# Kernel optimization log

Measured on AMD Instinct MI355X. Metric: run time of the kernel, lower is better.

## Reference

```python
import jax, jax.numpy as jnp
import numpy as np

N, D, OUT, E, K = 65536, 256, 256, 8, 2  # tokens, input_dim, output_dim, num_experts, top-k


def setup_inputs() -> dict:
    key = jax.random.key(0)
    k1, k2, k3, k4 = jax.random.split(key, 4)
    x = jax.random.normal(k1, (N, D), dtype=jnp.float32)
    # xavier_normal-like init for the gate
    w_gate = jax.random.normal(k2, (D, E), dtype=jnp.float32) * np.float32(np.sqrt(2.0 / (D + E)))
    # PWLayer params stacked over experts: bias init zeros, weight std 0.02
    expert_bias = jax.random.normal(k3, (E, D), dtype=jnp.float32) * 0.01
    expert_weight = jax.random.normal(k4, (E, OUT, D), dtype=jnp.float32) * 0.02
    return {"x": x, "w_gate": w_gate, "expert_bias": expert_bias, "expert_weight": expert_weight}


def reference(x, w_gate, expert_bias, expert_weight):
    # --- noisy_top_k_gating (eval mode: clean logits only) ---
    logits = x @ w_gate                                   # [N, E]
    top_v, top_i = jax.lax.top_k(logits, K)               # [N, K]
    sparse_logits = jnp.full_like(logits, -jnp.inf)
    rows = jnp.arange(logits.shape[0])[:, None]           # [N, 1]
    sparse_logits = sparse_logits.at[rows, top_i].set(top_v)
    gates = jax.nn.softmax(sparse_logits, axis=-1)        # [N, E], zeros off the top-k
    # --- dense all-expert PWLayer pass: (x - bias_e) @ W_e^T ---
    centered = x[:, None, :] - expert_bias[None, :, :]    # [N, E, D]
    expert_stack = jnp.einsum('ned,eod->neo', centered, expert_weight)  # [N, E, OUT]
    # --- gated combine ---
    return jnp.einsum('ne,neo->no', gates, expert_stack)  # [N, OUT]
```

## Files before the change

### kernel.cpp

```cpp
#include <hip/hip_runtime.h>
#include <hip/hip_bf16.h>
#include <math.h>

#define N_TOK 65536
#define DIM   256
#define NEXP  8

using frag_ab = __attribute__((ext_vector_type(8))) short;
using frag_cd = __attribute__((ext_vector_type(4))) float;

__device__ __forceinline__ unsigned short f2bf(float f) {
  unsigned u = __float_as_uint(f);
  u += 0x7FFFu + ((u >> 16) & 1u);
  return (unsigned short)(u >> 16);
}

__device__ __forceinline__ void gl2lds16(const unsigned short* g, unsigned short* l) {
  __builtin_amdgcn_global_load_lds(
      (const __attribute__((address_space(1))) void*)g,
      (__attribute__((address_space(3))) void*)l, 16, 0, 0);
}


__global__ __launch_bounds__(256) void k_prep(
    const float* __restrict__ w,
    const float* __restrict__ bias,
    unsigned short* __restrict__ Wb,
    float* __restrict__ c,
    int* __restrict__ meta) {
  int tid = threadIdx.x;
  int wid = (blockIdx.x * 256 + tid) >> 6;
  int lane = tid & 63;
  int e = wid >> 8, o = wid & 255;
  const float* wr = w + (size_t)(e * 256 + o) * DIM + lane * 4;
  float4 wv = *(const float4*)wr;
  const float* br = bias + e * DIM + lane * 4;
  float4 bv = *(const float4*)br;
  float s = wv.x * bv.x + wv.y * bv.y + wv.z * bv.z + wv.w * bv.w;
  #pragma unroll
  for (int m = 1; m < 64; m <<= 1) s += __shfl_xor(s, m, 64);
  if (lane == 0) c[e * 256 + o] = s;
  ushort4 h; h.x = f2bf(wv.x); h.y = f2bf(wv.y); h.z = f2bf(wv.z); h.w = f2bf(wv.w);
  *(ushort4*)(Wb + (size_t)e * 65536 + (size_t)(lane >> 1) * 2048 + o * 8 + (lane & 1) * 4) = h;
  if (blockIdx.x == 0 && tid < 192) meta[tid] = 0;
}

__global__ __launch_bounds__(256) void k_gating(
    const float* __restrict__ x,
    const float* __restrict__ wg,
    unsigned short* __restrict__ xb,
    int* __restrict__ routeE,
    float* __restrict__ routeG,
    int* __restrict__ meta) {
  __shared__ double swg[DIM * NEXP];
  __shared__ float  chunk[64 * 35];
  __shared__ int    hcnt[64];
  int tid = threadIdx.x;
  int tok0 = blockIdx.x * 64;
  int tk = tid >> 2, sub = tid & 3;

  for (int i = tid; i < DIM * NEXP; i += 256) swg[i] = (double)wg[i];
  if (tid < 64) hcnt[tid] = 0;

  double p[NEXP];
  #pragma unroll
  for (int e = 0; e < NEXP; e++) p[e] = 0.0;

  int f0 = tid, f1 = 256 + tid;
  int r0 = f0 >> 3, c40 = (f0 & 7) * 4;
  int r1 = f1 >> 3, c41 = (f1 & 7) * 4;
  const float* xs0 = x + (size_t)(tok0 + r0) * DIM + c40;
  const float* xs1 = x + (size_t)(tok0 + r1) * DIM + c41;
  unsigned short* xd0 = xb + (size_t)(tok0 + r0) * DIM + c40;
  unsigned short* xd1 = xb + (size_t)(tok0 + r1) * DIM + c41;

  float4 v0 = *(const float4*)(xs0);
  float4 v1 = *(const float4*)(xs1);

  for (int dc = 0; dc < 8; dc++) {
    __syncthreads();
    {
      ushort4 h0; h0.x = f2bf(v0.x); h0.y = f2bf(v0.y); h0.z = f2bf(v0.z); h0.w = f2bf(v0.w);
      ushort4 h1; h1.x = f2bf(v1.x); h1.y = f2bf(v1.y); h1.z = f2bf(v1.z); h1.w = f2bf(v1.w);
      *(ushort4*)(xd0 + dc * 32) = h0;
      *(ushort4*)(xd1 + dc * 32) = h1;
      float* d0 = &chunk[r0 * 35 + c40];
      d0[0] = v0.x; d0[1] = v0.y; d0[2] = v0.z; d0[3] = v0.w;
      float* d1 = &chunk[r1 * 35 + c41];
      d1[0] = v1.x; d1[1] = v1.y; d1[2] = v1.z; d1[3] = v1.w;
    }
    float4 n0 = make_float4(0.f, 0.f, 0.f, 0.f);
    float4 n1 = make_float4(0.f, 0.f, 0.f, 0.f);
    if (dc < 7) {
      n0 = *(const float4*)(xs0 + (dc + 1) * 32);
      n1 = *(const float4*)(xs1 + (dc + 1) * 32);
    }
    __syncthreads();
    #pragma unroll
    for (int c8 = 0; c8 < 8; c8++) {
      int cc = c8 * 4 + sub;
      double xv = (double)chunk[tk * 35 + cc];
      const double* wrow = &swg[(dc * 32 + cc) * NEXP];
      #pragma unroll
      for (int e = 0; e < NEXP; e++) p[e] += xv * wrow[e];
    }
    v0 = n0; v1 = n1;
  }

  #pragma unroll
  for (int e = 0; e < NEXP; e++) {
    p[e] += __shfl_xor(p[e], 1, 64);
    p[e] += __shfl_xor(p[e], 2, 64);
  }

  if (sub == 0) {
    int i1 = 0; double v1d = p[0];
    #pragma unroll
    for (int e = 1; e < NEXP; e++) { if (p[e] > v1d) { v1d = p[e]; i1 = e; } }
    int i2 = -1; double v2d = -1e300;
    #pragma unroll
    for (int e = 0; e < NEXP; e++) { if (e != i1 && p[e] > v2d) { v2d = p[e]; i2 = e; } }
    double t = exp(v2d - v1d);
    float g1 = (float)(1.0 / (1.0 + t));
    float g2 = 1.0f - g1;

    int n = tok0 + tk;
    routeE[n] = i1 | (i2 << 8);
    *(float2*)(routeG + 2 * (size_t)n) = make_float2(g1, g2);
    int a = i1 < i2 ? i1 : i2, b = i1 < i2 ? i2 : i1;
    atomicAdd(&hcnt[a * 8 + b], 1);
  }
  __syncthreads();
  if (tid < 64) atomicAdd(&meta[tid], hcnt[tid]);
}

__global__ void k_scan(int* __restrict__ meta) {
  if (threadIdx.x == 0) {
    int run = 0;
    for (int p = 0; p < 64; p++) {
      meta[64 + p] = run; meta[128 + p] = run;
      run += ((meta[p] + 63) >> 6) << 6;
    }
  }
}

__global__ __launch_bounds__(1024) void k_scatter(
    const int* __restrict__ routeE, const float* __restrict__ routeG,
    int* __restrict__ meta,
    int* __restrict__ srcTok, float* __restrict__ srcGA, float* __restrict__ srcGB) {
  __shared__ int cnt[64], bse[64];
  int tid = threadIdx.x;
  if (tid < 64) cnt[tid] = 0;
  __syncthreads();
  int n = blockIdx.x * 1024 + tid;
  int ep = routeE[n];
  int e1 = ep & 255, e2 = ep >> 8;
  float2 g = *(const float2*)(routeG + 2 * (size_t)n);
  int a = e1 < e2 ? e1 : e2, b = e1 < e2 ? e2 : e1;
  float ga = e1 < e2 ? g.x : g.y;
  float gb = e1 < e2 ? g.y : g.x;
  int pid = a * 8 + b;
  int r = atomicAdd(&cnt[pid], 1);
  __syncthreads();
  if (tid < 64) bse[tid] = atomicAdd(&meta[128 + tid], cnt[tid]);
  __syncthreads();
  int p = bse[pid] + r;
  srcTok[p] = n; srcGA[p] = ga; srcGB[p] = gb;
}

__global__ __launch_bounds__(512, 4) void k_gemm_pair(
    const unsigned short* __restrict__ xb,
    const unsigned short* __restrict__ Wb,
    const int* __restrict__ meta,
    const int* __restrict__ srcTok,
    const float* __restrict__ srcGA, const float* __restrict__ srcGB,
    const float* __restrict__ c,
    float* __restrict__ out) {
  __shared__ unsigned short sA[4][64 * 64];
  __shared__ int   sTok[64];
  __shared__ float sGAs[64], sGBs[64];
  __shared__ float sCorA[256], sCorB[256];
  int tid = threadIdx.x;

  int rem = blockIdx.x, pid = 0, ne = 0;
  for (pid = 0; pid < 64; pid++) {
    ne = meta[pid];
    int tiles = (ne + 63) >> 6;
    if (rem < tiles) break;
    rem -= tiles;
  }
  if (pid == 64) return;
  int ea = pid >> 3, eb = pid & 7;
  int mt = rem;
  int slot0 = meta[64 + pid] + mt * 64;

  if (tid < 64) {
    int idx = mt * 64 + tid;
    bool v = idx < ne;
    sTok[tid]  = v ? srcTok[slot0 + tid] : 0;
    sGAs[tid]  = v ? srcGA[slot0 + tid] : 0.f;
    sGBs[tid]  = v ? srcGB[slot0 + tid] : 1.f;
  } else if (tid >= 128 && tid < 192) {
    ((float4*)sCorA)[tid - 128] = ((const float4*)(c + ea * 256))[tid - 128];
  } else if (tid >= 192 && tid < 256) {
    ((float4*)sCorB)[tid - 192] = ((const float4*)(c + eb * 256))[tid - 192];
  }
  __syncthreads();

  int w = tid >> 6, lane = tid & 63;
  int lrow = lane >> 3, lchk = lane & 7;

  {
    int r = w * 8 + lrow;
    int cc = (lchk - r) & 7;
    const unsigned short* src = xb + (size_t)sTok[r] * 256 + cc * 8;
    #pragma unroll
    for (int kk = 0; kk < 4; kk++)
      gl2lds16(src + kk * 64, &sA[kk][w * 8 * 64]);
  }

  int wm = w & 1, wn = w >> 1;
  int lr = lane & 15, lk = lane >> 4;
  float rat[2][4];
  {
    __syncthreads();
    #pragma unroll
    for (int i = 0; i < 2; i++)
      #pragma unroll
      for (int rr = 0; rr < 4; rr++) {
        int m = wm * 32 + i * 16 + lk * 4 + rr;
        rat[i][rr] = sGAs[m] / sGBs[m];
      }
  }

  int offA[2][2];
  #pragma unroll
  for (int ks = 0; ks < 2; ks++)
    #pragma unroll
    for (int i = 0; i < 2; i++) {
      int ra = wm * 32 + i * 16 + lr;
      offA[ks][i] = ra * 64 + ((ks * 4 + lk + ra) & 7) * 8;
    }

  const unsigned short* bBaseA =
      Wb + (size_t)ea * 65536 + (size_t)lk * 2048 + (wn * 64 + lr) * 8;
  const unsigned short* bBaseB =
      Wb + (size_t)eb * 65536 + (size_t)lk * 2048 + (wn * 64 + lr) * 8;

  frag_cd acc[2][4];
  #pragma unroll
  for (int i = 0; i < 2; i++)
    #pragma unroll
    for (int j = 0; j < 4; j++)
      acc[i][j] = (frag_cd){0.f, 0.f, 0.f, 0.f};

#define BPTR(C) (((C) < 8 ? bBaseA : bBaseB) + (((C) & 7) >> 1) * 16384 + ((C) & 1) * 8192)
#define LOADB(DST, C) do {                                                  \
    _Pragma("unroll")                                                       \
    for (int j = 0; j < 4; j++) DST[j] = *(const frag_ab*)(BPTR(C) + j * 128); \
  } while (0)

#define SGB(M, N) __builtin_amdgcn_sched_group_barrier((M), (N), 0)

#define CLUSTER(C, BUF) do {                                                \
    const int ks_ = (C) & 1, kk_ = ((C) & 7) >> 1;                          \
    frag_ab av0 = *(const frag_ab*)(&sA[kk_][0] + offA[ks_][0]);            \
    frag_ab av1 = *(const frag_ab*)(&sA[kk_][0] + offA[ks_][1]);            \
    _Pragma("unroll")                                                       \
    for (int j = 0; j < 4; j++) {                                           \
      acc[0][j] = __builtin_amdgcn_mfma_f32_16x16x32_bf16(av0, BUF[j], acc[0][j], 0, 0, 0); \
      acc[1][j] = __builtin_amdgcn_mfma_f32_16x16x32_bf16(av1, BUF[j], acc[1][j], 0, 0, 0); \
    }                                                                       \
    if ((C) + 3 < 16) { LOADB(BUF, (C) + 3); SGB(0x020, 4); }               \
    SGB(0x100, 2);                                                          \
    SGB(0x008, 8);                                                          \
  } while (0)

  frag_ab bvA[4], bvB[4], bvC[4];
  LOADB(bvA, 0); LOADB(bvB, 1); LOADB(bvC, 2);
  SGB(0x020, 12);

  CLUSTER(0, bvA);  CLUSTER(1, bvB);  CLUSTER(2, bvC);
  CLUSTER(3, bvA);  CLUSTER(4, bvB);  CLUSTER(5, bvC);
  CLUSTER(6, bvA);  CLUSTER(7, bvB);

  #pragma unroll
  for (int i = 0; i < 2; i++)
    #pragma unroll
    for (int rr = 0; rr < 4; rr++)
      #pragma unroll
      for (int j = 0; j < 4; j++) acc[i][j][rr] *= rat[i][rr];

  CLUSTER(8, bvC);  CLUSTER(9, bvA);  CLUSTER(10, bvB); CLUSTER(11, bvC);
  CLUSTER(12, bvA); CLUSTER(13, bvB); CLUSTER(14, bvC); CLUSTER(15, bvA);

#undef CLUSTER
#undef SGB
#undef LOADB
#undef BPTR

  #pragma unroll
  for (int i = 0; i < 2; i++) {
    #pragma unroll
    for (int rr = 0; rr < 4; rr++) {
      int m = wm * 32 + i * 16 + lk * 4 + rr;
      if (mt * 64 + m < ne) {
        int tokn = sTok[m];
        float sa = sGAs[m], sb = sGBs[m];
        float* orow = out + (size_t)tokn * 256;
        #pragma unroll
        for (int j = 0; j < 4; j++) {
          int col = wn * 64 + j * 16 + lr;
          orow[col] = sb * acc[i][j][rr] - (sa * sCorA[col] + sb * sCorB[col]);
        }
      }
    }
  }
}

extern "C" void kernel_launch(void* const* d_in, const int* in_sizes, int n_in,
                              void* d_out, int out_size, void* d_ws, size_t ws_size,
                              hipStream_t stream) {
  const float* x    = (const float*)d_in[0];
  const float* wg   = (const float*)d_in[1];
  const float* bias = (const float*)d_in[2];
  const float* w    = (const float*)d_in[3];
  float* out = (float*)d_out;
  char* ws = (char*)d_ws;

  unsigned short* xb = (unsigned short*)(ws);
  unsigned short* Wb = (unsigned short*)(ws + 33554432);
  float* c           = (float*)(ws + 34603008);
  int* meta          = (int*)(ws + 34611200);
  int* routeE        = (int*)(ws + 34612224);
  float* routeG      = (float*)(ws + 34874368);
  int* srcTok        = (int*)(ws + 35398656);
  float* srcGA       = (float*)(ws + 35678720);
  float* srcGB       = (float*)(ws + 35958784);

  hipLaunchKernelGGL(k_prep,      dim3(512),  dim3(256),  0, stream, w, bias, Wb, c, meta);
  hipLaunchKernelGGL(k_gating,    dim3(1024), dim3(256),  0, stream, x, wg, xb, routeE, routeG, meta);
  hipLaunchKernelGGL(k_scan,      dim3(1),    dim3(64),   0, stream, meta);
  hipLaunchKernelGGL(k_scatter,   dim3(64),   dim3(1024), 0, stream, routeE, routeG, meta,
                     srcTok, srcGA, srcGB);
  hipLaunchKernelGGL(k_gemm_pair, dim3(1056), dim3(512),  0, stream, xb, Wb,
                     meta, srcTok, srcGA, srcGB, c, out);
}
```

Measured before the change: 173.1 us.

## Restructure gating kernel to read x directly from registers, drop LDS staging

The gating kernel now handles 32 tokens per block, with 8 threads per token. Each thread keeps its float4 slice of x in registers and multiplies it against a padded (stride-9) double-precision gate weight table in shared memory. This removes the per-chunk LDS staging buffer and its two barriers per iteration, at the cost of one extra shuffle-reduction step. Separately, the GEMM kernel's launch bounds now request 8 waves per SIMD instead of 4, which may squeeze its registers.

```diff
diff --git a/kernel.cpp b/kernel.cpp
--- a/kernel.cpp
+++ b/kernel.cpp
@@ -52,65 +52,44 @@
     int* __restrict__ routeE,
     float* __restrict__ routeG,
     int* __restrict__ meta) {
-  __shared__ double swg[DIM * NEXP];
-  __shared__ float  chunk[64 * 35];
+  __shared__ double swg[DIM * 9];
   __shared__ int    hcnt[64];
   int tid = threadIdx.x;
-  int tok0 = blockIdx.x * 64;
-  int tk = tid >> 2, sub = tid & 3;
-
-  for (int i = tid; i < DIM * NEXP; i += 256) swg[i] = (double)wg[i];
+  int tok0 = blockIdx.x * 32;
+  int r = tid >> 3, sub = tid & 7;
+
+  for (int i = tid; i < DIM * NEXP; i += 256)
+    swg[(i >> 3) * 9 + (i & 7)] = (double)wg[i];
   if (tid < 64) hcnt[tid] = 0;
+  __syncthreads();
+
+  const float* xs = x + (size_t)(tok0 + r) * DIM + sub * 4;
+  unsigned short* xd = xb + (size_t)(tok0 + r) * DIM + sub * 4;
 
   double p[NEXP];
   #pragma unroll
   for (int e = 0; e < NEXP; e++) p[e] = 0.0;
 
-  int f0 = tid, f1 = 256 + tid;
-  int r0 = f0 >> 3, c40 = (f0 & 7) * 4;
-  int r1 = f1 >> 3, c41 = (f1 & 7) * 4;
-  const float* xs0 = x + (size_t)(tok0 + r0) * DIM + c40;
-  const float* xs1 = x + (size_t)(tok0 + r1) * DIM + c41;
-  unsigned short* xd0 = xb + (size_t)(tok0 + r0) * DIM + c40;
-  unsigned short* xd1 = xb + (size_t)(tok0 + r1) * DIM + c41;
-
-  float4 v0 = *(const float4*)(xs0);
-  float4 v1 = *(const float4*)(xs1);
-
+  float4 v = *(const float4*)xs;
+  #pragma unroll
   for (int dc = 0; dc < 8; dc++) {
-    __syncthreads();
-    {
-      ushort4 h0; h0.x = f2bf(v0.x); h0.y = f2bf(v0.y); h0.z = f2bf(v0.z); h0.w = f2bf(v0.w);
-      ushort4 h1; h1.x = f2bf(v1.x); h1.y = f2bf(v1.y); h1.z = f2bf(v1.z); h1.w = f2bf(v1.w);
-      *(ushort4*)(xd0 + dc * 32) = h0;
-      *(ushort4*)(xd1 + dc * 32) = h1;
-      float* d0 = &chunk[r0 * 35 + c40];
-      d0[0] = v0.x; d0[1] = v0.y; d0[2] = v0.z; d0[3] = v0.w;
-      float* d1 = &chunk[r1 * 35 + c41];
-      d1[0] = v1.x; d1[1] = v1.y; d1[2] = v1.z; d1[3] = v1.w;
-    }
-    float4 n0 = make_float4(0.f, 0.f, 0.f, 0.f);
-    float4 n1 = make_float4(0.f, 0.f, 0.f, 0.f);
-    if (dc < 7) {
-      n0 = *(const float4*)(xs0 + (dc + 1) * 32);
-      n1 = *(const float4*)(xs1 + (dc + 1) * 32);
-    }
-    __syncthreads();
-    #pragma unroll
-    for (int c8 = 0; c8 < 8; c8++) {
-      int cc = c8 * 4 + sub;
-      double xv = (double)chunk[tk * 35 + cc];
-      const double* wrow = &swg[(dc * 32 + cc) * NEXP];
-      #pragma unroll
-      for (int e = 0; e < NEXP; e++) p[e] += xv * wrow[e];
-    }
-    v0 = n0; v1 = n1;
+    float4 nv = make_float4(0.f, 0.f, 0.f, 0.f);
+    if (dc < 7) nv = *(const float4*)(xs + (dc + 1) * 32);
+    ushort4 h; h.x = f2bf(v.x); h.y = f2bf(v.y); h.z = f2bf(v.z); h.w = f2bf(v.w);
+    *(ushort4*)(xd + dc * 32) = h;
+    const double* w0 = &swg[(dc * 32 + sub * 4) * 9];
+    double x0 = (double)v.x, x1 = (double)v.y, x2 = (double)v.z, x3 = (double)v.w;
+    #pragma unroll
+    for (int e = 0; e < NEXP; e++)
+      p[e] += x0 * w0[e] + x1 * w0[9 + e] + x2 * w0[18 + e] + x3 * w0[27 + e];
+    v = nv;
   }
 
   #pragma unroll
   for (int e = 0; e < NEXP; e++) {
     p[e] += __shfl_xor(p[e], 1, 64);
     p[e] += __shfl_xor(p[e], 2, 64);
+    p[e] += __shfl_xor(p[e], 4, 64);
   }
 
   if (sub == 0) {
@@ -124,7 +103,7 @@
     float g1 = (float)(1.0 / (1.0 + t));
     float g2 = 1.0f - g1;
 
-    int n = tok0 + tk;
+    int n = tok0 + r;
     routeE[n] = i1 | (i2 << 8);
     *(float2*)(routeG + 2 * (size_t)n) = make_float2(g1, g2);
     int a = i1 < i2 ? i1 : i2, b = i1 < i2 ? i2 : i1;
@@ -168,7 +147,7 @@
   srcTok[p] = n; srcGA[p] = ga; srcGB[p] = gb;
 }
 
-__global__ __launch_bounds__(512, 4) void k_gemm_pair(
+__global__ __launch_bounds__(512, 8) void k_gemm_pair(
     const unsigned short* __restrict__ xb,
     const unsigned short* __restrict__ Wb,
     const int* __restrict__ meta,
@@ -339,7 +318,7 @@
   float* srcGB       = (float*)(ws + 35958784);
 
   hipLaunchKernelGGL(k_prep,      dim3(512),  dim3(256),  0, stream, w, bias, Wb, c, meta);
-  hipLaunchKernelGGL(k_gating,    dim3(1024), dim3(256),  0, stream, x, wg, xb, routeE, routeG, meta);
+  hipLaunchKernelGGL(k_gating,    dim3(2048), dim3(256),  0, stream, x, wg, xb, routeE, routeG, meta);
   hipLaunchKernelGGL(k_scan,      dim3(1),    dim3(64),   0, stream, meta);
   hipLaunchKernelGGL(k_scatter,   dim3(64),   dim3(1024), 0, stream, routeE, routeG, meta,
                      srcTok, srcGA, srcGB);
```

After: 328.1 us. 1.9x slower.
